# Performance work log

Hardware: AMD Instinct MI355X
Metric: run time of the kernel (lower is better)

## Reference

```python
import jax, jax.numpy as jnp
import numpy as np
from jax import lax

K = 3          # kernel size
STRIDE = 1
PAD = 1
DIL = 1


def setup_inputs() -> dict:
    key = jax.random.key(0)
    ks = jax.random.split(key, 6)
    B, C, H, W = 4, 64, 128, 128
    OFF_C = 32
    x = jax.random.normal(ks[0], (B, C, H, W), dtype=jnp.float32)
    offset_feat = jax.random.normal(ks[1], (B, OFF_C, H, W), dtype=jnp.float32)
    # offset/mask conv params (module inits to zero; use small random values so
    # the deformable sampling path is actually exercised)
    w_off = jax.random.normal(ks[2], (3 * K * K, OFF_C, K, K), dtype=jnp.float32) * 0.05
    b_off = jnp.zeros((3 * K * K,), dtype=jnp.float32)
    # main conv weight: uniform(-stdv, stdv), stdv = 1/sqrt(C*K*K)
    stdv = 1.0 / np.sqrt(C * K * K)
    weight = jax.random.uniform(ks[3], (C, C, K, K), dtype=jnp.float32, minval=-stdv, maxval=stdv)
    bias = jnp.zeros((C,), dtype=jnp.float32)
    return {"x": x, "offset_feat": offset_feat, "w_off": w_off, "b_off": b_off,
            "weight": weight, "bias": bias}


def _deform_conv2d(x, offset, mask, weight, bias):
    """Modulated deformable conv, deformable_groups=1, groups=1.
    x:      [B, C, H, W]
    offset: [B, 2*K*K, Ho, Wo]  (torchvision layout: ch 2k = dy_k, 2k+1 = dx_k)
    mask:   [B, K*K, Ho, Wo]    (already sigmoided)
    weight: [O, C, K, K]
    """
    B, C, H, W = x.shape
    K2 = mask.shape[1]
    Ho, Wo = mask.shape[2], mask.shape[3]
    off = offset.reshape(B, K2, 2, Ho, Wo)
    dy, dx = off[:, :, 0], off[:, :, 1]              # [B, K2, Ho, Wo]

    ky = jnp.repeat(jnp.arange(K), K).astype(jnp.float32)   # [K2] row-major
    kx = jnp.tile(jnp.arange(K), K).astype(jnp.float32)
    base_y = (jnp.arange(Ho, dtype=jnp.float32) * STRIDE - PAD)[None, :, None] + (ky * DIL)[:, None, None]
    base_x = (jnp.arange(Wo, dtype=jnp.float32) * STRIDE - PAD)[None, None, :] + (kx * DIL)[:, None, None]
    py = base_y[None] + dy                           # [B, K2, Ho, Wo]
    px = base_x[None] + dx

    def sample_one(img, py_b, px_b):
        # img [C, H, W]; py_b/px_b [K2, Ho, Wo] -> [C, K2, Ho, Wo]
        y0 = jnp.floor(py_b)
        x0 = jnp.floor(px_b)
        wy1 = py_b - y0
        wx1 = px_b - x0

        def gather(yi, xi):
            valid = (yi >= 0) & (yi <= H - 1) & (xi >= 0) & (xi <= W - 1)
            yc = jnp.clip(yi, 0, H - 1).astype(jnp.int32)
            xc = jnp.clip(xi, 0, W - 1).astype(jnp.int32)
            return img[:, yc, xc] * valid[None].astype(img.dtype)

        v00 = gather(y0, x0)
        v01 = gather(y0, x0 + 1)
        v10 = gather(y0 + 1, x0)
        v11 = gather(y0 + 1, x0 + 1)
        return ((1 - wy1) * ((1 - wx1) * v00 + wx1 * v01)
                + wy1 * ((1 - wx1) * v10 + wx1 * v11))

    sampled = jax.vmap(sample_one)(x, py, px)        # [B, C, K2, Ho, Wo]
    sampled = sampled * mask[:, None]                # modulation
    w2 = weight.reshape(weight.shape[0], C, K2)      # k = i*K + j row-major
    out = jnp.einsum('bckhw,ock->bohw', sampled, w2)
    if bias is not None:
        out = out + bias[None, :, None, None]
    return out


def reference(x, offset_feat, w_off, b_off, weight, bias):
    # offset/mask conv (standard 3x3, stride 1, pad 1)
    om = lax.conv_general_dilated(
        offset_feat, w_off, window_strides=(STRIDE, STRIDE),
        padding=[(PAD, PAD), (PAD, PAD)],
        rhs_dilation=(1, 1),
        dimension_numbers=('NCHW', 'OIHW', 'NCHW'))
    om = om + b_off[None, :, None, None]
    o1, o2, mask = jnp.split(om, 3, axis=1)
    offset = jnp.concatenate([o1, o2], axis=1)       # [B, 2*K*K, Ho, Wo]
    mask = jax.nn.sigmoid(mask)
    return _deform_conv2d(x, offset, mask, weight, bias)
```

## Files before the change

kernel.cpp:

```cpp
#include <hip/hip_runtime.h>
#include <math.h>

typedef unsigned short ushort_t;
typedef unsigned int uint_t;
typedef __attribute__((ext_vector_type(8))) short short8;
typedef __attribute__((ext_vector_type(4))) float f32x4;

#define NB 4
#define NC 64
#define NH 128
#define NW 128
#define OFFC 32


__device__ __forceinline__ void async_copy16(void* lds_dst, const void* g_src) {
    __builtin_amdgcn_global_load_lds(
        (const __attribute__((address_space(1))) unsigned int*)g_src,
        (__attribute__((address_space(3))) unsigned int*)lds_dst, 16, 0, 0);
}

__device__ __forceinline__ void split_bf16(float v, ushort_t& h, ushort_t& l) {
    uint_t bb = __float_as_uint(v);
    uint_t rr = bb + 0x7fffu + ((bb >> 16) & 1u);
    h = (ushort_t)(rr >> 16);
    float hf = __uint_as_float(((uint_t)h) << 16);
    float lof = v - hf;
    l = (ushort_t)(__float_as_uint(lof) >> 16);
}

__global__ __launch_bounds__(256) void prep_weights(
        const float* __restrict__ weight, const float* __restrict__ w_off,
        ushort_t* __restrict__ g_wbh, ushort_t* __restrict__ g_wbl,
        float* __restrict__ wt_off) {
    int idx = blockIdx.x * 256 + threadIdx.x;
    if (idx < 9 * 64 * 72) {
        int k   = idx % 72;
        int o   = (idx / 72) % 64;
        int tap = idx / (72 * 64);
        float v = (k < 64) ? weight[(o * 64 + k) * 9 + tap] : 0.0f;
        ushort_t h, l;
        split_bf16(v, h, l);
        g_wbh[idx] = h;
        g_wbl[idx] = l;
    }
    int idx2 = idx - 9 * 64 * 72;
    if (idx2 >= 0 && idx2 < 32 * 9 * 28) {
        int oc  = idx2 % 28;
        int r   = idx2 / 28;
        int tap = r % 9;
        int ic  = r / 9;
        wt_off[idx2] = (oc < 27) ? w_off[(oc * 32 + ic) * 9 + tap] : 0.0f;
    }
}

__global__ __launch_bounds__(256) void transpose_x(
        const float* __restrict__ x, float* __restrict__ xt) {
    __shared__ float lds[64][130];
    int b = blockIdx.x >> 7;
    int y = blockIdx.x & 127;
    int t = threadIdx.x;
    int xx = t & 127;
    int c0 = t >> 7;
#pragma unroll
    for (int it = 0; it < 32; ++it) {
        int c = it * 2 + c0;
        lds[c][xx] = x[((b * 64 + c) * 128 + y) * 128 + xx];
    }
    __syncthreads();
#pragma unroll
    for (int it = 0; it < 32; ++it) {
        int flat = it * 256 + t;
        int c  = flat & 63;
        int x2 = flat >> 6;
        xt[((b * 128 + y) * 128 + x2) * 64 + c] = lds[c][x2];
    }
}

__global__ __launch_bounds__(256) void offset_conv(
        const float* __restrict__ feat, const float* __restrict__ wt_off,
        const float* __restrict__ b_off, uint_t* __restrict__ coefA) {
    __shared__ float red[4][27][64];
    int wv = threadIdx.x >> 6, lane = threadIdx.x & 63;
    int pix = blockIdx.x * 64 + lane;
    int b = pix >> 14, y = (pix >> 7) & 127, x = pix & 127;
    float acc[27];
#pragma unroll
    for (int o = 0; o < 27; ++o) acc[o] = 0.0f;
    for (int ic = wv * 8; ic < wv * 8 + 8; ++ic) {
        float v[9];
#pragma unroll
        for (int kh = 0; kh < 3; ++kh) {
#pragma unroll
            for (int kw = 0; kw < 3; ++kw) {
                int yy = y - 1 + kh;
                int xx = x - 1 + kw;
                float valid = (yy >= 0 && yy < NH && xx >= 0 && xx < NW) ? 1.0f : 0.0f;
                int yyc = min(max(yy, 0), NH - 1);
                int xxc = min(max(xx, 0), NW - 1);
                v[kh * 3 + kw] = feat[((b * OFFC + ic) * NH + yyc) * NW + xxc] * valid;
            }
        }
#pragma unroll
        for (int tap = 0; tap < 9; ++tap)
#pragma unroll
            for (int o = 0; o < 27; ++o)
                acc[o] = fmaf(v[tap], wt_off[(ic * 9 + tap) * 28 + o], acc[o]);
    }
#pragma unroll
    for (int o = 0; o < 27; ++o) red[wv][o][lane] = acc[o];
    __syncthreads();
    for (int t = wv; t < 9; t += 4) {
        float dy = red[0][2 * t][lane] + red[1][2 * t][lane]
                 + red[2][2 * t][lane] + red[3][2 * t][lane] + b_off[2 * t];
        float dx = red[0][2 * t + 1][lane] + red[1][2 * t + 1][lane]
                 + red[2][2 * t + 1][lane] + red[3][2 * t + 1][lane] + b_off[2 * t + 1];
        float mv = red[0][18 + t][lane] + red[1][18 + t][lane]
                 + red[2][18 + t][lane] + red[3][18 + t][lane] + b_off[18 + t];
        float mm = 1.0f / (1.0f + __expf(-mv));
        float py  = (float)(y - 1 + t / 3) + dy;
        float pxf = (float)(x - 1 + t % 3) + dx;
        float y0f = floorf(py), x0f = floorf(pxf);
        float wy = py - y0f, wx = pxf - x0f;
        int iy0 = (int)y0f, ix0 = (int)x0f;
        int iy1 = iy0 + 1, ix1 = ix0 + 1;
        float vy0 = (iy0 >= 0 && iy0 < NH) ? 1.0f : 0.0f;
        float vy1 = (iy1 >= 0 && iy1 < NH) ? 1.0f : 0.0f;
        float vx0 = (ix0 >= 0 && ix0 < NW) ? 1.0f : 0.0f;
        float vx1 = (ix1 >= 0 && ix1 < NW) ? 1.0f : 0.0f;
        int iy0c = min(max(iy0, 0), NH - 1), iy1c = min(max(iy1, 0), NH - 1);
        int ix0c = min(max(ix0, 0), NW - 1), ix1c = min(max(ix1, 0), NW - 1);
        float c00 = (1.0f - wy) * (1.0f - wx) * vy0 * vx0 * mm;
        float c01 = (1.0f - wy) * wx * vy0 * vx1 * mm;
        float c10 = wy * (1.0f - wx) * vy1 * vx0 * mm;
        float c11 = wy * wx * vy1 * vx1 * mm;
        uint_t u00 = (__float_as_uint(c00) & ~127u) | (uint_t)iy0c;
        uint_t u01 = (__float_as_uint(c01) & ~127u) | (uint_t)iy1c;
        uint_t u10 = (__float_as_uint(c10) & ~127u) | (uint_t)ix0c;
        uint_t u11 = (__float_as_uint(c11) & ~127u) | (uint_t)ix1c;
        *(uint4*)&coefA[((size_t)t * 65536 + pix) * 4] = make_uint4(u00, u01, u10, u11);
    }
}

__global__ __launch_bounds__(512, 4) void deform_main(
        const float* __restrict__ xt, const uint_t* __restrict__ coefA,
        const ushort_t* __restrict__ g_wbh, const ushort_t* __restrict__ g_wbl,
        const float* __restrict__ bias, float* __restrict__ out) {
    __shared__ __align__(16) ushort_t s_hi[128][72];
    __shared__ __align__(16) ushort_t s_lo[128][72];
    __shared__ __align__(16) ushort_t wb[2][2][64][72];

    int w = threadIdx.x >> 6, lane = threadIdx.x & 63;
    int col = lane & 15;
    int kgrp = lane >> 4;
    int blk = (blockIdx.x & 7) * 64 + (blockIdx.x >> 3);
    int b = blk >> 7, y = blk & 127;
    int pix0 = blk * 128;
    const float* xb = xt + (size_t)b * (NH * NW * NC);

    f32x4 acc[4];
#pragma unroll
    for (int n = 0; n < 4; ++n) {
        float bv = bias[n * 16 + col];
        acc[n] = (f32x4){bv, bv, bv, bv};
    }

    auto prefetchW = [&](int tap, int bi) {
        for (int j = w; j < 18; j += 8) {
            int hsel = (j < 9) ? 0 : 1;
            int j2 = (j < 9) ? j : j - 9;
            const ushort_t* src = (hsel ? g_wbl : g_wbh) + tap * 4608 + j2 * 512 + lane * 8;
            ushort_t* dst = &wb[bi][hsel][0][0] + j2 * 512;
            async_copy16(dst, src);
        }
    };

    prefetchW(0, 0);
    __syncthreads();

    for (int t = 0; t < 9; ++t) {
#pragma unroll 4
        for (int p = 0; p < 16; ++p) {
            int rowi = w * 16 + p;
            int px = pix0 + rowi;
            uint4 cu = *(const uint4*)&coefA[((size_t)t * 65536 + px) * 4];
            float c00 = __uint_as_float(cu.x), c01 = __uint_as_float(cu.y);
            float c10 = __uint_as_float(cu.z), c11 = __uint_as_float(cu.w);
            int r0 = (int)(cu.x & 127u) << 13;
            int r1 = (int)(cu.y & 127u) << 13;
            int q0 = (int)(cu.z & 127u) << 6;
            int q1 = (int)(cu.w & 127u) << 6;
            float v00 = xb[r0 + q0 + lane];
            float v01 = xb[r0 + q1 + lane];
            float v10 = xb[r1 + q0 + lane];
            float v11 = xb[r1 + q1 + lane];
            float s = c00 * v00 + c01 * v01 + c10 * v10 + c11 * v11;
            ushort_t h, l;
            split_bf16(s, h, l);
            s_hi[rowi][lane] = h;
            s_lo[rowi][lane] = l;
        }
        if (t < 8) prefetchW(t + 1, (t + 1) & 1);
        __syncthreads();

        {
            int bi = t & 1;
            short8 ah[2], al[2];
#pragma unroll
            for (int ks = 0; ks < 2; ++ks) {
                int row = w * 16 + col;
                ah[ks] = *(const short8*)&s_hi[row][ks * 32 + kgrp * 8];
                al[ks] = *(const short8*)&s_lo[row][ks * 32 + kgrp * 8];
            }
#pragma unroll
            for (int h = 0; h < 2; ++h) {
                short8 bh[2][2], bl[2][2];
#pragma unroll
                for (int n2 = 0; n2 < 2; ++n2)
#pragma unroll
                    for (int ks = 0; ks < 2; ++ks) {
                        int o = (h * 2 + n2) * 16 + col;
                        bh[n2][ks] = *(const short8*)&wb[bi][0][o][ks * 32 + kgrp * 8];
                        bl[n2][ks] = *(const short8*)&wb[bi][1][o][ks * 32 + kgrp * 8];
                    }
#pragma unroll
                for (int n2 = 0; n2 < 2; ++n2) {
                    int n = h * 2 + n2;
                    acc[n] = __builtin_amdgcn_mfma_f32_16x16x32_bf16(ah[0], bh[n2][0], acc[n], 0, 0, 0);
                    acc[n] = __builtin_amdgcn_mfma_f32_16x16x32_bf16(ah[1], bh[n2][1], acc[n], 0, 0, 0);
                    acc[n] = __builtin_amdgcn_mfma_f32_16x16x32_bf16(ah[0], bl[n2][0], acc[n], 0, 0, 0);
                    acc[n] = __builtin_amdgcn_mfma_f32_16x16x32_bf16(ah[1], bl[n2][1], acc[n], 0, 0, 0);
                    acc[n] = __builtin_amdgcn_mfma_f32_16x16x32_bf16(al[0], bh[n2][0], acc[n], 0, 0, 0);
                    acc[n] = __builtin_amdgcn_mfma_f32_16x16x32_bf16(al[1], bh[n2][1], acc[n], 0, 0, 0);
                }
            }
        }
        __syncthreads();
    }

#pragma unroll
    for (int n = 0; n < 4; ++n) {
        int o = n * 16 + col;
        int x = w * 16 + kgrp * 4;
        float* dst = out + (((size_t)(b * 64 + o)) * 128 + y) * 128 + x;
        *(f32x4*)dst = acc[n];
    }
}

extern "C" void kernel_launch(void* const* d_in, const int* in_sizes, int n_in,
                              void* d_out, int out_size, void* d_ws, size_t ws_size,
                              hipStream_t stream) {
    const float* x        = (const float*)d_in[0];
    const float* off_feat = (const float*)d_in[1];
    const float* w_off    = (const float*)d_in[2];
    const float* b_off    = (const float*)d_in[3];
    const float* weight   = (const float*)d_in[4];
    const float* bias     = (const float*)d_in[5];
    float* out = (float*)d_out;

    float* ws      = (float*)d_ws;
    float* xt      = ws;
    uint_t* coefA  = (uint_t*)(ws + 4194304);
    float* wt_off  = ws + 6553600;
    ushort_t* g_wbh = (ushort_t*)(ws + 6561664);
    ushort_t* g_wbl = (ushort_t*)(ws + 6582400);

    prep_weights<<<194, 256, 0, stream>>>(weight, w_off, g_wbh, g_wbl, wt_off);
    transpose_x<<<512, 256, 0, stream>>>(x, xt);
    offset_conv<<<1024, 256, 0, stream>>>(off_feat, wt_off, b_off, coefA);
    deform_main<<<512, 512, 0, stream>>>(xt, coefA, g_wbh, g_wbl, bias, out);
}
```

Measured before the change: 220.8 us.

## Fuse transpose and offset conv kernels; load coefficients once per wave via readlane

Merges the x transpose and offset-conv kernels into one launch that branches on block index, removing a launch and letting the two independent jobs overlap. In the main kernel each wave now loads its 16 pixels' packed coefficients with one coalesced load and broadcasts them through readlane, rather than issuing uniform uint4 loads per pixel. It also fully unrolls the sampling loop and replaces the rounded bf16 hi/lo split with a truncating split. The truncating split changes rounding slightly, and the full unroll raises register pressure.

Result: faster. 193.3 us (-12.5%).

```diff
diff --git a/kernel.cpp b/kernel.cpp
--- a/kernel.cpp
+++ b/kernel.cpp
@@ -53,35 +53,37 @@
     }
 }
 
-__global__ __launch_bounds__(256) void transpose_x(
-        const float* __restrict__ x, float* __restrict__ xt) {
-    __shared__ float lds[64][130];
-    int b = blockIdx.x >> 7;
-    int y = blockIdx.x & 127;
-    int t = threadIdx.x;
-    int xx = t & 127;
-    int c0 = t >> 7;
-#pragma unroll
-    for (int it = 0; it < 32; ++it) {
-        int c = it * 2 + c0;
-        lds[c][xx] = x[((b * 64 + c) * 128 + y) * 128 + xx];
-    }
-    __syncthreads();
-#pragma unroll
-    for (int it = 0; it < 32; ++it) {
-        int flat = it * 256 + t;
-        int c  = flat & 63;
-        int x2 = flat >> 6;
-        xt[((b * 128 + y) * 128 + x2) * 64 + c] = lds[c][x2];
-    }
-}
-
-__global__ __launch_bounds__(256) void offset_conv(
+__global__ __launch_bounds__(256) void aux_fused(
+        const float* __restrict__ xin, float* __restrict__ xt,
         const float* __restrict__ feat, const float* __restrict__ wt_off,
         const float* __restrict__ b_off, uint_t* __restrict__ coefA) {
-    __shared__ float red[4][27][64];
-    int wv = threadIdx.x >> 6, lane = threadIdx.x & 63;
-    int pix = blockIdx.x * 64 + lane;
+    __shared__ __align__(16) float smem[8320];
+    int bid = blockIdx.x;
+    int t = threadIdx.x;
+    if (bid < 512) {
+        float (*lds)[130] = (float (*)[130])smem;
+        int b = bid >> 7;
+        int y = bid & 127;
+        int xx = t & 127;
+        int c0 = t >> 7;
+#pragma unroll
+        for (int it = 0; it < 32; ++it) {
+            int c = it * 2 + c0;
+            lds[c][xx] = xin[((b * 64 + c) * 128 + y) * 128 + xx];
+        }
+        __syncthreads();
+#pragma unroll
+        for (int it = 0; it < 32; ++it) {
+            int flat = it * 256 + t;
+            int c  = flat & 63;
+            int x2 = flat >> 6;
+            xt[((b * 128 + y) * 128 + x2) * 64 + c] = lds[c][x2];
+        }
+        return;
+    }
+    float (*red)[27][64] = (float (*)[27][64])smem;
+    int wv = t >> 6, lane = t & 63;
+    int pix = (bid - 512) * 64 + lane;
     int b = pix >> 14, y = (pix >> 7) & 127, x = pix & 127;
     float acc[27];
 #pragma unroll
@@ -109,16 +111,16 @@
 #pragma unroll
     for (int o = 0; o < 27; ++o) red[wv][o][lane] = acc[o];
     __syncthreads();
-    for (int t = wv; t < 9; t += 4) {
-        float dy = red[0][2 * t][lane] + red[1][2 * t][lane]
-                 + red[2][2 * t][lane] + red[3][2 * t][lane] + b_off[2 * t];
-        float dx = red[0][2 * t + 1][lane] + red[1][2 * t + 1][lane]
-                 + red[2][2 * t + 1][lane] + red[3][2 * t + 1][lane] + b_off[2 * t + 1];
-        float mv = red[0][18 + t][lane] + red[1][18 + t][lane]
-                 + red[2][18 + t][lane] + red[3][18 + t][lane] + b_off[18 + t];
+    for (int tp = wv; tp < 9; tp += 4) {
+        float dy = red[0][2 * tp][lane] + red[1][2 * tp][lane]
+                 + red[2][2 * tp][lane] + red[3][2 * tp][lane] + b_off[2 * tp];
+        float dx = red[0][2 * tp + 1][lane] + red[1][2 * tp + 1][lane]
+                 + red[2][2 * tp + 1][lane] + red[3][2 * tp + 1][lane] + b_off[2 * tp + 1];
+        float mv = red[0][18 + tp][lane] + red[1][18 + tp][lane]
+                 + red[2][18 + tp][lane] + red[3][18 + tp][lane] + b_off[18 + tp];
         float mm = 1.0f / (1.0f + __expf(-mv));
-        float py  = (float)(y - 1 + t / 3) + dy;
-        float pxf = (float)(x - 1 + t % 3) + dx;
+        float py  = (float)(y - 1 + tp / 3) + dy;
+        float pxf = (float)(x - 1 + tp % 3) + dx;
         float y0f = floorf(py), x0f = floorf(pxf);
         float wy = py - y0f, wx = pxf - x0f;
         int iy0 = (int)y0f, ix0 = (int)x0f;
@@ -137,7 +139,7 @@
         uint_t u01 = (__float_as_uint(c01) & ~127u) | (uint_t)iy1c;
         uint_t u10 = (__float_as_uint(c10) & ~127u) | (uint_t)ix0c;
         uint_t u11 = (__float_as_uint(c11) & ~127u) | (uint_t)ix1c;
-        *(uint4*)&coefA[((size_t)t * 65536 + pix) * 4] = make_uint4(u00, u01, u10, u11);
+        *(uint4*)&coefA[((size_t)tp * 65536 + pix) * 4] = make_uint4(u00, u01, u10, u11);
     }
 }
 
@@ -149,7 +151,8 @@
     __shared__ __align__(16) ushort_t s_lo[128][72];
     __shared__ __align__(16) ushort_t wb[2][2][64][72];
 
-    int w = threadIdx.x >> 6, lane = threadIdx.x & 63;
+    int lane = threadIdx.x & 63;
+    int wu = __builtin_amdgcn_readfirstlane(threadIdx.x >> 6);
     int col = lane & 15;
     int kgrp = lane >> 4;
     int blk = (blockIdx.x & 7) * 64 + (blockIdx.x >> 3);
@@ -165,7 +168,7 @@
     }
 
     auto prefetchW = [&](int tap, int bi) {
-        for (int j = w; j < 18; j += 8) {
+        for (int j = wu; j < 18; j += 8) {
             int hsel = (j < 9) ? 0 : 1;
             int j2 = (j < 9) ? j : j - 9;
             const ushort_t* src = (hsel ? g_wbl : g_wbh) + tap * 4608 + j2 * 512 + lane * 8;
@@ -178,26 +181,38 @@
     __syncthreads();
 
     for (int t = 0; t < 9; ++t) {
-#pragma unroll 4
+        uint_t cw = coefA[((size_t)t * 65536 + pix0) * 4 + wu * 64 + lane];
+#pragma unroll
         for (int p = 0; p < 16; ++p) {
-            int rowi = w * 16 + p;
-            int px = pix0 + rowi;
-            uint4 cu = *(const uint4*)&coefA[((size_t)t * 65536 + px) * 4];
-            float c00 = __uint_as_float(cu.x), c01 = __uint_as_float(cu.y);
-            float c10 = __uint_as_float(cu.z), c11 = __uint_as_float(cu.w);
-            int r0 = (int)(cu.x & 127u) << 13;
-            int r1 = (int)(cu.y & 127u) << 13;
-            int q0 = (int)(cu.z & 127u) << 6;
-            int q1 = (int)(cu.w & 127u) << 6;
-            float v00 = xb[r0 + q0 + lane];
-            float v01 = xb[r0 + q1 + lane];
-            float v10 = xb[r1 + q0 + lane];
-            float v11 = xb[r1 + q1 + lane];
-            float s = c00 * v00 + c01 * v01 + c10 * v10 + c11 * v11;
-            ushort_t h, l;
-            split_bf16(s, h, l);
-            s_hi[rowi][lane] = h;
-            s_lo[rowi][lane] = l;
+            uint_t u00 = (uint_t)__builtin_amdgcn_readlane((int)cw, 4 * p + 0);
+            uint_t u01 = (uint_t)__builtin_amdgcn_readlane((int)cw, 4 * p + 1);
+            uint_t u10 = (uint_t)__builtin_amdgcn_readlane((int)cw, 4 * p + 2);
+            uint_t u11 = (uint_t)__builtin_amdgcn_readlane((int)cw, 4 * p + 3);
+            float c00 = __uint_as_float(u00 & ~127u);
+            float c01 = __uint_as_float(u01 & ~127u);
+            float c10 = __uint_as_float(u10 & ~127u);
+            float c11 = __uint_as_float(u11 & ~127u);
+            const float* r0 = xb + ((u00 & 127u) << 13);
+            const float* r1 = xb + ((u01 & 127u) << 13);
+            uint_t q0 = (u10 & 127u) << 6;
+            uint_t q1 = (u11 & 127u) << 6;
+            const float* p00 = r0 + q0;
+            const float* p01 = r0 + q1;
+            const float* p10 = r1 + q0;
+            const float* p11 = r1 + q1;
+            float v00 = p00[lane];
+            float v01 = p01[lane];
+            float v10 = p10[lane];
+            float v11 = p11[lane];
+            float s = c00 * v00;
+            s = fmaf(c01, v01, s);
+            s = fmaf(c10, v10, s);
+            s = fmaf(c11, v11, s);
+            uint_t sb = __float_as_uint(s);
+            float lof = s - __uint_as_float(sb & 0xffff0000u);
+            int rowi = wu * 16 + p;
+            s_hi[rowi][lane] = (ushort_t)(sb >> 16);
+            s_lo[rowi][lane] = (ushort_t)(__float_as_uint(lof) >> 16);
         }
         if (t < 8) prefetchW(t + 1, (t + 1) & 1);
         __syncthreads();
@@ -207,7 +222,7 @@
             short8 ah[2], al[2];
 #pragma unroll
             for (int ks = 0; ks < 2; ++ks) {
-                int row = w * 16 + col;
+                int row = wu * 16 + col;
                 ah[ks] = *(const short8*)&s_hi[row][ks * 32 + kgrp * 8];
                 al[ks] = *(const short8*)&s_lo[row][ks * 32 + kgrp * 8];
             }
@@ -240,7 +255,7 @@
 #pragma unroll
     for (int n = 0; n < 4; ++n) {
         int o = n * 16 + col;
-        int x = w * 16 + kgrp * 4;
+        int x = wu * 16 + kgrp * 4;
         float* dst = out + (((size_t)(b * 64 + o)) * 128 + y) * 128 + x;
         *(f32x4*)dst = acc[n];
     }
@@ -265,7 +280,6 @@
     ushort_t* g_wbl = (ushort_t*)(ws + 6582400);
 
     prep_weights<<<194, 256, 0, stream>>>(weight, w_off, g_wbh, g_wbl, wt_off);
-    transpose_x<<<512, 256, 0, stream>>>(x, xt);
-    offset_conv<<<1024, 256, 0, stream>>>(off_feat, wt_off, b_off, coefA);
+    aux_fused<<<1536, 256, 0, stream>>>(x, xt, off_feat, wt_off, b_off, coefA);
     deform_main<<<512, 512, 0, stream>>>(xt, coefA, g_wbh, g_wbl, bias, out);
 }
```
